# Optimization experiments

Hardware: AMD Instinct MI355X
Metric: run time of the kernel (lower is better)

## Reference

```python
import jax, jax.numpy as jnp
import numpy as np

EPS = 1.1920929e-07  # torch RMSNorm default eps = float32 finfo eps

def rms_norm(x, w):
    return x * jax.lax.rsqrt(jnp.mean(x * x, axis=-1, keepdims=True) + EPS) * w

def setup_inputs() -> dict:
    key = jax.random.key(0)
    ks = jax.random.split(key, 10)
    B, C, H, W = 8, 64, 48, 48
    E = C  # embed_dim = query_dim = key_dim = value_dim
    q = jax.random.normal(ks[0], (B, C, H, W), jnp.float32)
    k = jax.random.normal(ks[1], (B, C, H, W), jnp.float32)
    v = jax.random.normal(ks[2], (B, C, H, W), jnp.float32)
    s = 1.0 / np.sqrt(E)
    conv_w = jax.random.normal(ks[3], (C, C, 3, 3), jnp.float32) * (1.0 / np.sqrt(C * 9))
    nq_w = jnp.ones((E,), jnp.float32)
    nk_w = jnp.ones((E,), jnp.float32)
    wq = jax.random.normal(ks[4], (E, E), jnp.float32) * s
    bq = jax.random.normal(ks[5], (E,), jnp.float32) * 0.01
    wk = jax.random.normal(ks[6], (E, E), jnp.float32) * s
    bk = jax.random.normal(ks[7], (E,), jnp.float32) * 0.01
    return {"q": q, "k": k, "v": v, "conv_w": conv_w, "nq_w": nq_w,
            "nk_w": nk_w, "wq": wq, "bq": bq, "wk": wk, "bk": bk}

def reference(q, k, v, conv_w, nq_w, nk_w, wq, bq, wk, bk):
    B, C, H, W = q.shape
    num_heads = 4
    head_dim = C // num_heads
    # conv2d 3x3, stride 1, same padding, no bias
    qc = jax.lax.conv_general_dilated(
        q, conv_w, window_strides=(1, 1), padding='SAME',
        dimension_numbers=('NCHW', 'OIHW', 'NCHW'))
    # b c h w -> b (h w) c
    qs = qc.reshape(B, C, H * W).transpose(0, 2, 1)
    ksq = k.reshape(B, C, -1).transpose(0, 2, 1)
    vsq = v.reshape(B, C, -1).transpose(0, 2, 1)
    # RMSNorm on q and k (norm_v output feeds MHA value path whose output is discarded)
    qn = rms_norm(qs, nq_w)
    kn = rms_norm(ksq, nk_w)
    # MHA projections (q scaled by 1/sqrt(head_dim) as in torch)
    qp = (qn @ wq.T + bq) * (1.0 / np.sqrt(head_dim))
    kp = ksq_p = kn @ wk.T + bk
    Sq, Sk = qp.shape[1], kp.shape[1]
    qh = qp.reshape(B, Sq, num_heads, head_dim)
    kh = kp.reshape(B, Sk, num_heads, head_dim)
    scores = jnp.einsum('bihd,bjhd->bhij', qh, kh)
    attn = jax.nn.softmax(scores, axis=-1)
    # average_attn_weights=True -> mean over heads
    attn_avg = jnp.mean(attn, axis=1)  # [b, i, j]
    # custom output: weighted sum over RAW (un-normed, unprojected) value
    out = jnp.einsum('bij,bjd->bid', attn_avg, vsq)
    return out
```

## Files before the change

### kernel.cpp

```cpp
#include <hip/hip_runtime.h>
#include <hip/hip_bf16.h>

namespace {
constexpr int kB = 8;
constexpr int kC = 64;
constexpr int kH = 48;
constexpr int kW = 48;
constexpr int kS = kH * kW;
constexpr float kEps = 1.1920929e-07f;
}

typedef __attribute__((ext_vector_type(8))) short short8;
typedef __attribute__((ext_vector_type(4))) short short4_t;
typedef __attribute__((ext_vector_type(4))) float f32x4;

__device__ __forceinline__ short f2bf(float x) {
  unsigned u = __float_as_uint(x);
  u += 0x7fffu + ((u >> 16) & 1u);
  return (short)(u >> 16);
}
__device__ __forceinline__ float bf2f(short s) {
  return __uint_as_float(((unsigned)(unsigned short)s) << 16);
}

__global__ __launch_bounds__(256) void fused_prep(
    const float* __restrict__ q, const float* __restrict__ k,
    const float* __restrict__ v, const float* __restrict__ wq,
    const float* __restrict__ wk, const float* __restrict__ conv_w,
    short* __restrict__ qt, short* __restrict__ kt, short* __restrict__ vt,
    short* __restrict__ wqb3, short* __restrict__ wkb3, short* __restrict__ wt3) {
  const int blk = blockIdx.x;
  if (blk < 576) {
    __shared__ float tile[64][65];
    const int zz = blk / 36;
    const int bx = blk % 36;
    const int b = zz >> 1;
    const float* src = (zz & 1) ? k : q;
    short* dst = (zz & 1) ? kt : qt;
    const int s0 = bx * 64;
    const int tx = threadIdx.x & 63;
    const int ty = threadIdx.x >> 6;
#pragma unroll
    for (int r = 0; r < 16; ++r) {
      int c = r * 4 + ty;
      tile[c][tx] = src[((size_t)b * kC + c) * kS + s0 + tx];
    }
    __syncthreads();
#pragma unroll
    for (int r = 0; r < 16; ++r) {
      int s = r * 4 + ty;
      dst[((size_t)b * kS + s0 + s) * kC + tx] = f2bf(tile[tx][s]);
    }
  } else if (blk < 1728) {
    int idx = ((blk - 576) * 256 + threadIdx.x) * 4;
    float4 x = *reinterpret_cast<const float4*>(v + idx);
    int2 o;
    o.x = ((int)(unsigned short)f2bf(x.y) << 16) | (unsigned short)f2bf(x.x);
    o.y = ((int)(unsigned short)f2bf(x.w) << 16) | (unsigned short)f2bf(x.z);
    *reinterpret_cast<int2*>(vt + idx) = o;
  } else {
    int idx = (blk - 1728) * 256 + threadIdx.x;
    if (idx < 4096) {
      int j = idx & 7, Lw = (idx >> 3) & 63, slab = idx >> 9;
      int nt = slab & 3, kh = slab >> 2;
      int e = nt * 16 + (Lw & 15), c = kh * 32 + (Lw >> 4) * 8 + j;
      wqb3[idx] = f2bf(wq[e * 64 + c]);
    } else if (idx < 8192) {
      int i2 = idx - 4096;
      int j = i2 & 7, Lw = (i2 >> 3) & 63, slab = i2 >> 9;
      int nt = slab & 3, kh = slab >> 2;
      int e = nt * 16 + (Lw & 15), c = kh * 32 + (Lw >> 4) * 8 + j;
      wkb3[i2] = f2bf(wk[e * 64 + c]);
    } else {
      int i3 = idx - 8192;
      int j = i3 & 7, Lw = (i3 >> 3) & 63, slab = i3 >> 9;
      int nt = slab & 3, kh = (slab >> 2) & 1, tap = slab >> 3;
      int co = nt * 16 + (Lw & 15), ci = kh * 32 + (Lw >> 4) * 8 + j;
      wt3[i3] = f2bf(conv_w[co * 576 + ci * 9 + tap]);
    }
  }
}

__global__ __launch_bounds__(256) void fused_qk_gemm(
    const short* __restrict__ qt, const short* __restrict__ kt,
    const short* __restrict__ wt3, const short* __restrict__ wqb3,
    const short* __restrict__ wkb3,
    const float* __restrict__ nq_w, const float* __restrict__ nk_w,
    const float* __restrict__ bq, const float* __restrict__ bk,
    short* __restrict__ qp, short* __restrict__ kp) {
  __shared__ __align__(16) short Qs[164][72];
  __shared__ __align__(16) short ln[4][16][80];
  const int blk = blockIdx.x;
  const int t = threadIdx.x;
  const int ws = t >> 6;
  const int L = t & 63;
  const int quad = L >> 4;
  const int l16 = L & 15;
  const short8 zero8 = {0, 0, 0, 0, 0, 0, 0, 0};

  if (blk < 288) {
    const int b = blk / 36;
    const int S0 = (blk % 36) * 64;
    const int sBase = S0 + ws * 16;
    const int s = sBase + l16;
    const int h = s / kW, w = s % kW;

    const short* qtb = qt + (size_t)b * kS * kC;
#pragma unroll
    for (int it = 0; it < 6; ++it) {
      int idx = it * 256 + t;
      if (idx < 164 * 8) {
        int r = idx >> 3, sg = idx & 7;
        int srow = S0 - 49 + r;
        srow = srow < 0 ? 0 : (srow >= kS ? kS - 1 : srow);
        *reinterpret_cast<int4*>(&Qs[r][sg * 8]) =
            *reinterpret_cast<const int4*>(qtb + (size_t)srow * kC + sg * 8);
      }
    }
    __syncthreads();

    const int baseLocal = ws * 16 + l16 + 49;
    f32x4 acc[4] = {{0.f, 0.f, 0.f, 0.f}, {0.f, 0.f, 0.f, 0.f},
                    {0.f, 0.f, 0.f, 0.f}, {0.f, 0.f, 0.f, 0.f}};
#pragma unroll
    for (int tap = 0; tap < 9; ++tap) {
      const int dh = tap / 3 - 1, dw = tap % 3 - 1;
      const bool valid = (unsigned)(h + dh) < (unsigned)kH &&
                         (unsigned)(w + dw) < (unsigned)kW;
      const int local = baseLocal + dh * kW + dw;
#pragma unroll
      for (int kh = 0; kh < 2; ++kh) {
        short8 af = *reinterpret_cast<const short8*>(&Qs[local][kh * 32 + quad * 8]);
        af = valid ? af : zero8;
        const short* wb = wt3 + ((tap * 2 + kh) * 4) * 512 + L * 8;
#pragma unroll
        for (int nt = 0; nt < 4; ++nt) {
          short8 bf = *reinterpret_cast<const short8*>(wb + nt * 512);
          acc[nt] = __builtin_amdgcn_mfma_f32_16x16x32_bf16(af, bf, acc[nt], 0, 0, 0);
        }
      }
    }
    float rstd[4];
#pragma unroll
    for (int reg = 0; reg < 4; ++reg) {
      float pr = acc[0][reg] * acc[0][reg] + acc[1][reg] * acc[1][reg]
               + acc[2][reg] * acc[2][reg] + acc[3][reg] * acc[3][reg];
      pr += __shfl_xor(pr, 1, 64);
      pr += __shfl_xor(pr, 2, 64);
      pr += __shfl_xor(pr, 4, 64);
      pr += __shfl_xor(pr, 8, 64);
      rstd[reg] = rsqrtf(pr * (1.0f / kC) + kEps);
    }
#pragma unroll
    for (int nt = 0; nt < 4; ++nt) {
      float g = nq_w[nt * 16 + l16];
#pragma unroll
      for (int reg = 0; reg < 4; ++reg) {
        ln[ws][quad * 4 + reg][nt * 16 + l16] = f2bf(acc[nt][reg] * rstd[reg] * g);
      }
    }
    __syncthreads();
    f32x4 acc2[4] = {{0.f, 0.f, 0.f, 0.f}, {0.f, 0.f, 0.f, 0.f},
                     {0.f, 0.f, 0.f, 0.f}, {0.f, 0.f, 0.f, 0.f}};
#pragma unroll
    for (int kh = 0; kh < 2; ++kh) {
      short8 af = *reinterpret_cast<const short8*>(&ln[ws][l16][kh * 32 + quad * 8]);
      const short* wb = wqb3 + (kh * 4) * 512 + L * 8;
#pragma unroll
      for (int nt = 0; nt < 4; ++nt) {
        short8 bf = *reinterpret_cast<const short8*>(wb + nt * 512);
        acc2[nt] = __builtin_amdgcn_mfma_f32_16x16x32_bf16(af, bf, acc2[nt], 0, 0, 0);
      }
    }
#pragma unroll
    for (int nt = 0; nt < 4; ++nt) {
      const int e = nt * 16 + l16;
      float bias = bq[e];
#pragma unroll
      for (int reg = 0; reg < 4; ++reg) {
        qp[((size_t)b * kS + sBase + quad * 4 + reg) * kC + e] =
            f2bf((acc2[nt][reg] + bias) * 0.36067376022224085f);
      }
    }
  } else {
    const int idx = blk - 288;
    const int b = idx / 36;
    const int S0 = (idx % 36) * 64;
    const int sBase = S0 + ws * 16;

    const short* ktb = kt + ((size_t)b * kS + S0) * kC;
#pragma unroll
    for (int it = 0; it < 2; ++it) {
      int r = it * 32 + (t >> 3), sg = t & 7;
      *reinterpret_cast<int4*>(&Qs[r][sg * 8]) =
          *reinterpret_cast<const int4*>(ktb + (size_t)r * kC + sg * 8);
    }
    __syncthreads();

    short8 af0 = *reinterpret_cast<const short8*>(&Qs[ws * 16 + l16][quad * 8]);
    short8 af1 = *reinterpret_cast<const short8*>(&Qs[ws * 16 + l16][32 + quad * 8]);

    float xs[16];
#pragma unroll
    for (int j = 0; j < 8; ++j) { xs[j] = bf2f(af0[j]); xs[8 + j] = bf2f(af1[j]); }
    float sum = 0.f;
#pragma unroll
    for (int j = 0; j < 16; ++j) sum = fmaf(xs[j], xs[j], sum);
    sum += __shfl_xor(sum, 16, 64);
    sum += __shfl_xor(sum, 32, 64);
    float rstd = rsqrtf(sum * (1.0f / kC) + kEps);

    const float* n0 = nk_w + quad * 8;
#pragma unroll
    for (int j = 0; j < 8; ++j) {
      af0[j] = f2bf(xs[j] * rstd * n0[j]);
      af1[j] = f2bf(xs[8 + j] * rstd * n0[32 + j]);
    }

    f32x4 acc[4] = {{0.f, 0.f, 0.f, 0.f}, {0.f, 0.f, 0.f, 0.f},
                    {0.f, 0.f, 0.f, 0.f}, {0.f, 0.f, 0.f, 0.f}};
#pragma unroll
    for (int nt = 0; nt < 4; ++nt) {
      short8 bf0 = *reinterpret_cast<const short8*>(
          wkb3 + (0 * 4 + nt) * 512 + L * 8);
      short8 bf1 = *reinterpret_cast<const short8*>(
          wkb3 + (1 * 4 + nt) * 512 + L * 8);
      acc[nt] = __builtin_amdgcn_mfma_f32_16x16x32_bf16(af0, bf0, acc[nt], 0, 0, 0);
      acc[nt] = __builtin_amdgcn_mfma_f32_16x16x32_bf16(af1, bf1, acc[nt], 0, 0, 0);
    }
#pragma unroll
    for (int nt = 0; nt < 4; ++nt) {
      const int e = nt * 16 + l16;
      float bias = bk[e];
#pragma unroll
      for (int reg = 0; reg < 4; ++reg) {
        kp[((size_t)b * kS + sBase + quad * 4 + reg) * kC + e] =
            f2bf(acc[nt][reg] + bias);
      }
    }
  }
}

__global__ __launch_bounds__(256, 4) void attn_flash(
    const short* __restrict__ qp, const short* __restrict__ kp,
    const short* __restrict__ vt, float* __restrict__ out) {
  __shared__ __align__(16) char pool[2 * 64 * 72 * 2 + 2 * 64 * 76 * 2];
  __shared__ float pl[4][16][4];
  __shared__ float Li[16][4];

  short (*Kt)[64][72] = reinterpret_cast<short (*)[64][72]>(pool);
  short (*Vt)[64][76] = reinterpret_cast<short (*)[64][76]>(pool + 2 * 64 * 72 * 2);
  float* slabF = reinterpret_cast<float*>(pool);

  const int blk = blockIdx.x;
  const int b = blk & 7;
  const int i0 = (blk >> 3) * 16;
  const int t = threadIdx.x;
  const int ws = t >> 6;
  const int L = t & 63;
  const int quad = L >> 4;
  const int l16 = L & 15;

  const f32x4 zc = {0.f, 0.f, 0.f, 0.f};

  const short* qrow = qp + ((size_t)b * kS + i0 + l16) * kC + quad * 4;
  short4_t qh[4];
#pragma unroll
  for (int h = 0; h < 4; ++h)
    qh[h] = *reinterpret_cast<const short4_t*>(qrow + h * 16);

  const int r8i = t >> 3;
  const int seg = t & 7;
  const short* kg = kp + (size_t)b * kS * kC;
  const short* vg = vt + (size_t)b * kC * kS;

  int4 kreg[2], vreg[2];
#pragma unroll
  for (int pass = 0; pass < 2; ++pass) {
    kreg[pass] = *reinterpret_cast<const int4*>(
        kg + (size_t)(pass * 32 + r8i) * kC + seg * 8);
    vreg[pass] = *reinterpret_cast<const int4*>(
        vg + (size_t)(pass * 32 + r8i) * kS + seg * 8);
  }
#pragma unroll
  for (int pass = 0; pass < 2; ++pass) {
    *reinterpret_cast<int4*>(&Kt[0][pass * 32 + r8i][seg * 8]) = kreg[pass];
    *reinterpret_cast<int4*>(&Vt[0][pass * 32 + r8i][seg * 8]) = vreg[pass];
  }
  __syncthreads();

  f32x4 U[4][4];
#pragma unroll
  for (int h = 0; h < 4; ++h)
#pragma unroll
    for (int d = 0; d < 4; ++d) U[h][d] = zc;
  float lh[4] = {0.f, 0.f, 0.f, 0.f};

  for (int jt = 0; jt < kS / 64; ++jt) {
    const int buf = jt & 1;
    const bool more = (jt + 1) < kS / 64;
    if (more) {
      const int jn = (jt + 1) * 64;
#pragma unroll
      for (int pass = 0; pass < 2; ++pass) {
        kreg[pass] = *reinterpret_cast<const int4*>(
            kg + (size_t)(jn + pass * 32 + r8i) * kC + seg * 8);
        vreg[pass] = *reinterpret_cast<const int4*>(
            vg + (size_t)(pass * 32 + r8i) * kS + jn + seg * 8);
      }
    }

    short4_t kf[4], vf[4];
#pragma unroll
    for (int h = 0; h < 4; ++h)
      kf[h] = *reinterpret_cast<const short4_t*>(
          &Kt[buf][ws * 16 + l16][h * 16 + quad * 4]);
#pragma unroll
    for (int d = 0; d < 4; ++d)
      vf[d] = *reinterpret_cast<const short4_t*>(
          &Vt[buf][d * 16 + l16][ws * 16 + quad * 4]);

    short4_t p[4];
#pragma unroll
    for (int h = 0; h < 4; ++h) {
      f32x4 s = __builtin_amdgcn_mfma_f32_16x16x16bf16_1k(kf[h], qh[h], zc, 0, 0, 0);
      float e0 = exp2f(s[0]), e1 = exp2f(s[1]);
      float e2 = exp2f(s[2]), e3 = exp2f(s[3]);
      lh[h] += (e0 + e1) + (e2 + e3);
      union { __hip_bfloat162 h2[2]; short4_t s4; } cv;
      cv.h2[0] = __float22bfloat162_rn(make_float2(e0, e1));
      cv.h2[1] = __float22bfloat162_rn(make_float2(e2, e3));
      p[h] = cv.s4;
    }
#pragma unroll
    for (int h = 0; h < 4; ++h)
#pragma unroll
      for (int d = 0; d < 4; ++d)
        U[h][d] = __builtin_amdgcn_mfma_f32_16x16x16bf16_1k(vf[d], p[h], U[h][d], 0, 0, 0);

    if (more) {
      const int nb = buf ^ 1;
#pragma unroll
      for (int pass = 0; pass < 2; ++pass) {
        *reinterpret_cast<int4*>(&Kt[nb][pass * 32 + r8i][seg * 8]) = kreg[pass];
        *reinterpret_cast<int4*>(&Vt[nb][pass * 32 + r8i][seg * 8]) = vreg[pass];
      }
    }
    __syncthreads();
  }

#pragma unroll
  for (int h = 0; h < 4; ++h) {
    lh[h] += __shfl_xor(lh[h], 16, 64);
    lh[h] += __shfl_xor(lh[h], 32, 64);
  }
  if (quad == 0) {
#pragma unroll
    for (int h = 0; h < 4; ++h) pl[ws][l16][h] = lh[h];
  }
  __syncthreads();
  if (t < 64) {
    const int i = t >> 2, h = t & 3;
    Li[i][h] = 0.25f / (pl[0][i][h] + pl[1][i][h] + pl[2][i][h] + pl[3][i][h]);
  }
  __syncthreads();
  float c[4];
#pragma unroll
  for (int h = 0; h < 4; ++h) c[h] = Li[l16][h];

#pragma unroll
  for (int d = 0; d < 4; ++d) {
    if (ws != 0) {
      const int sid = ws - 1;
#pragma unroll
      for (int h = 0; h < 4; ++h)
#pragma unroll
        for (int reg = 0; reg < 4; ++reg)
          slabF[((sid * 4 + h) * 4 + reg) * 66 + L] = U[h][d][reg];
    }
    __syncthreads();
    if (ws == 0) {
      float of[4] = {0.f, 0.f, 0.f, 0.f};
#pragma unroll
      for (int h = 0; h < 4; ++h) {
#pragma unroll
        for (int reg = 0; reg < 4; ++reg) {
          float tot = U[h][d][reg]
                    + slabF[((0 * 4 + h) * 4 + reg) * 66 + L]
                    + slabF[((1 * 4 + h) * 4 + reg) * 66 + L]
                    + slabF[((2 * 4 + h) * 4 + reg) * 66 + L];
          of[reg] += tot * c[h];
        }
      }
      *reinterpret_cast<float4*>(
          out + ((size_t)b * kS + i0 + l16) * kC + d * 16 + quad * 4) =
          make_float4(of[0], of[1], of[2], of[3]);
    }
    __syncthreads();
  }
}

extern "C" void kernel_launch(void* const* d_in, const int* in_sizes, int n_in,
                              void* d_out, int out_size, void* d_ws, size_t ws_size,
                              hipStream_t stream) {
  const float* q      = (const float*)d_in[0];
  const float* k      = (const float*)d_in[1];
  const float* v      = (const float*)d_in[2];
  const float* conv_w = (const float*)d_in[3];
  const float* nq_w   = (const float*)d_in[4];
  const float* nk_w   = (const float*)d_in[5];
  const float* wq     = (const float*)d_in[6];
  const float* bq     = (const float*)d_in[7];
  const float* wk     = (const float*)d_in[8];
  const float* bk     = (const float*)d_in[9];
  float* out = (float*)d_out;

  const size_t N = (size_t)kB * kS * kC;
  short* qt   = (short*)d_ws;
  short* kt   = qt + N;
  short* vt   = kt + N;
  short* qp   = vt + N;
  short* kp   = qp + N;
  short* wqb3 = kp + N;
  short* wkb3 = wqb3 + 4096;
  short* wt3  = wkb3 + 4096;

  fused_prep<<<1904, 256, 0, stream>>>(q, k, v, wq, wk, conv_w,
                                       qt, kt, vt, wqb3, wkb3, wt3);
  fused_qk_gemm<<<576, 256, 0, stream>>>(qt, kt, wt3, wqb3, wkb3,
                                         nq_w, nk_w, bq, bk, qp, kp);
  attn_flash<<<1152, 256, 0, stream>>>(qp, kp, vt, out);
}
```

Measured before the change: 176.6 us.

## Use 32-row query tiles with 16x16x32 MFMAs and an LDS-staged probability tile

The attention kernel now handles 32 query rows per block instead of 16, which halves the grid and reuses each K/V tile across twice as many queries. The wave split changes from four j-slices to two query subtiles by two j-halves. It switches to the K=32 bf16 MFMA, using zero-masked q fragments per head, and round-trips probabilities through LDS to re-layout them for the PV MFMA. The exp2 with a log2e prescale becomes __expf with a plain 0.25 scale. Occupancy drops to 3 blocks, and the extra LDS traffic plus the wasted half of each QK MFMA on zero-padded fragments add cost.

```diff
diff --git a/kernel.cpp b/kernel.cpp
--- a/kernel.cpp
+++ b/kernel.cpp
@@ -179,7 +179,7 @@
 #pragma unroll
       for (int reg = 0; reg < 4; ++reg) {
         qp[((size_t)b * kS + sBase + quad * 4 + reg) * kC + e] =
-            f2bf((acc2[nt][reg] + bias) * 0.36067376022224085f);
+            f2bf((acc2[nt][reg] + bias) * 0.25f);
       }
     }
   } else {
@@ -241,33 +241,38 @@
   }
 }
 
-__global__ __launch_bounds__(256, 4) void attn_flash(
+__global__ __launch_bounds__(256, 3) void attn_flash(
     const short* __restrict__ qp, const short* __restrict__ kp,
     const short* __restrict__ vt, float* __restrict__ out) {
-  __shared__ __align__(16) char pool[2 * 64 * 72 * 2 + 2 * 64 * 76 * 2];
+  __shared__ __align__(16) short Kt[2][64][72];
+  __shared__ __align__(16) short Vt[2][64][72];
+  __shared__ __align__(16) short ptile[4][16][40];
   __shared__ float pl[4][16][4];
-  __shared__ float Li[16][4];
-
-  short (*Kt)[64][72] = reinterpret_cast<short (*)[64][72]>(pool);
-  short (*Vt)[64][76] = reinterpret_cast<short (*)[64][76]>(pool + 2 * 64 * 72 * 2);
-  float* slabF = reinterpret_cast<float*>(pool);
+  __shared__ float Li[32][4];
+
+  float* slabF = reinterpret_cast<float*>(&Kt[0][0][0]);
 
   const int blk = blockIdx.x;
   const int b = blk & 7;
-  const int i0 = (blk >> 3) * 16;
+  const int i0 = (blk >> 3) * 32;
   const int t = threadIdx.x;
   const int ws = t >> 6;
+  const int isub = ws & 1;
+  const int jhalf = ws >> 1;
+  const int jbase = jhalf * 32;
   const int L = t & 63;
   const int quad = L >> 4;
   const int l16 = L & 15;
 
   const f32x4 zc = {0.f, 0.f, 0.f, 0.f};
-
-  const short* qrow = qp + ((size_t)b * kS + i0 + l16) * kC + quad * 4;
-  short4_t qh[4];
-#pragma unroll
-  for (int h = 0; h < 4; ++h)
-    qh[h] = *reinterpret_cast<const short4_t*>(qrow + h * 16);
+  const short8 z8 = {0, 0, 0, 0, 0, 0, 0, 0};
+
+  const short* qrow = qp + ((size_t)b * kS + i0 + isub * 16 + l16) * kC;
+  const short8 qw0 = *reinterpret_cast<const short8*>(qrow + quad * 8);
+  const short8 qw1 = *reinterpret_cast<const short8*>(qrow + 32 + quad * 8);
+  const bool lo = quad < 2;
+  const short8 qm[4] = {lo ? qw0 : z8, lo ? z8 : qw0,
+                        lo ? qw1 : z8, lo ? z8 : qw1};
 
   const int r8i = t >> 3;
   const int seg = t & 7;
@@ -310,33 +315,41 @@
       }
     }
 
-    short4_t kf[4], vf[4];
-#pragma unroll
-    for (int h = 0; h < 4; ++h)
-      kf[h] = *reinterpret_cast<const short4_t*>(
-          &Kt[buf][ws * 16 + l16][h * 16 + quad * 4]);
+    short8 kf[2][2];
+#pragma unroll
+    for (int c = 0; c < 2; ++c)
+#pragma unroll
+      for (int w = 0; w < 2; ++w)
+        kf[c][w] = *reinterpret_cast<const short8*>(
+            &Kt[buf][jbase + c * 16 + l16][w * 32 + quad * 8]);
+    short8 vf[4];
 #pragma unroll
     for (int d = 0; d < 4; ++d)
-      vf[d] = *reinterpret_cast<const short4_t*>(
-          &Vt[buf][d * 16 + l16][ws * 16 + quad * 4]);
-
-    short4_t p[4];
+      vf[d] = *reinterpret_cast<const short8*>(
+          &Vt[buf][d * 16 + l16][jbase + quad * 8]);
+
 #pragma unroll
     for (int h = 0; h < 4; ++h) {
-      f32x4 s = __builtin_amdgcn_mfma_f32_16x16x16bf16_1k(kf[h], qh[h], zc, 0, 0, 0);
-      float e0 = exp2f(s[0]), e1 = exp2f(s[1]);
-      float e2 = exp2f(s[2]), e3 = exp2f(s[3]);
-      lh[h] += (e0 + e1) + (e2 + e3);
-      union { __hip_bfloat162 h2[2]; short4_t s4; } cv;
-      cv.h2[0] = __float22bfloat162_rn(make_float2(e0, e1));
-      cv.h2[1] = __float22bfloat162_rn(make_float2(e2, e3));
-      p[h] = cv.s4;
-    }
-#pragma unroll
-    for (int h = 0; h < 4; ++h)
+      const int w = h >> 1;
+      f32x4 s0 = __builtin_amdgcn_mfma_f32_16x16x32_bf16(kf[0][w], qm[h], zc, 0, 0, 0);
+      f32x4 s1 = __builtin_amdgcn_mfma_f32_16x16x32_bf16(kf[1][w], qm[h], zc, 0, 0, 0);
+      float e0 = __expf(s0[0]), e1 = __expf(s0[1]);
+      float e2 = __expf(s0[2]), e3 = __expf(s0[3]);
+      float f0 = __expf(s1[0]), f1 = __expf(s1[1]);
+      float f2 = __expf(s1[2]), f3 = __expf(s1[3]);
+      lh[h] += ((e0 + e1) + (e2 + e3)) + ((f0 + f1) + (f2 + f3));
+      union { __hip_bfloat162 h2[2]; short4_t s4; } ca, cb;
+      ca.h2[0] = __float22bfloat162_rn(make_float2(e0, e1));
+      ca.h2[1] = __float22bfloat162_rn(make_float2(e2, e3));
+      cb.h2[0] = __float22bfloat162_rn(make_float2(f0, f1));
+      cb.h2[1] = __float22bfloat162_rn(make_float2(f2, f3));
+      *reinterpret_cast<short4_t*>(&ptile[ws][l16][quad * 4]) = ca.s4;
+      *reinterpret_cast<short4_t*>(&ptile[ws][l16][16 + quad * 4]) = cb.s4;
+      short8 pf = *reinterpret_cast<const short8*>(&ptile[ws][l16][quad * 8]);
 #pragma unroll
       for (int d = 0; d < 4; ++d)
-        U[h][d] = __builtin_amdgcn_mfma_f32_16x16x16bf16_1k(vf[d], p[h], U[h][d], 0, 0, 0);
+        U[h][d] = __builtin_amdgcn_mfma_f32_16x16x32_bf16(vf[d], pf, U[h][d], 0, 0, 0);
+    }
 
     if (more) {
       const int nb = buf ^ 1;
@@ -359,41 +372,37 @@
     for (int h = 0; h < 4; ++h) pl[ws][l16][h] = lh[h];
   }
   __syncthreads();
-  if (t < 64) {
+  if (t < 128) {
     const int i = t >> 2, h = t & 3;
-    Li[i][h] = 0.25f / (pl[0][i][h] + pl[1][i][h] + pl[2][i][h] + pl[3][i][h]);
+    Li[i][h] = 0.25f / (pl[i >> 4][i & 15][h] + pl[(i >> 4) + 2][i & 15][h]);
   }
   __syncthreads();
   float c[4];
 #pragma unroll
-  for (int h = 0; h < 4; ++h) c[h] = Li[l16][h];
+  for (int h = 0; h < 4; ++h) c[h] = Li[isub * 16 + l16][h];
 
 #pragma unroll
   for (int d = 0; d < 4; ++d) {
-    if (ws != 0) {
-      const int sid = ws - 1;
+    if (jhalf == 1) {
 #pragma unroll
       for (int h = 0; h < 4; ++h)
 #pragma unroll
         for (int reg = 0; reg < 4; ++reg)
-          slabF[((sid * 4 + h) * 4 + reg) * 66 + L] = U[h][d][reg];
-    }
-    __syncthreads();
-    if (ws == 0) {
+          slabF[((isub * 4 + h) * 4 + reg) * 66 + L] = U[h][d][reg];
+    }
+    __syncthreads();
+    if (jhalf == 0) {
       float of[4] = {0.f, 0.f, 0.f, 0.f};
 #pragma unroll
       for (int h = 0; h < 4; ++h) {
 #pragma unroll
         for (int reg = 0; reg < 4; ++reg) {
-          float tot = U[h][d][reg]
-                    + slabF[((0 * 4 + h) * 4 + reg) * 66 + L]
-                    + slabF[((1 * 4 + h) * 4 + reg) * 66 + L]
-                    + slabF[((2 * 4 + h) * 4 + reg) * 66 + L];
+          float tot = U[h][d][reg] + slabF[((isub * 4 + h) * 4 + reg) * 66 + L];
           of[reg] += tot * c[h];
         }
       }
       *reinterpret_cast<float4*>(
-          out + ((size_t)b * kS + i0 + l16) * kC + d * 16 + quad * 4) =
+          out + ((size_t)b * kS + i0 + isub * 16 + l16) * kC + d * 16 + quad * 4) =
           make_float4(of[0], of[1], of[2], of[3]);
     }
     __syncthreads();
@@ -429,5 +438,5 @@
                                        qt, kt, vt, wqb3, wkb3, wt3);
   fused_qk_gemm<<<576, 256, 0, stream>>>(qt, kt, wt3, wqb3, wkb3,
                                          nq_w, nk_w, bq, bk, qp, kp);
-  attn_flash<<<1152, 256, 0, stream>>>(qp, kp, vt, out);
-}
+  attn_flash<<<576, 256, 0, stream>>>(qp, kp, vt, out);
+}
```

New measurement: 162.7 us. 1.09x faster.
